# Kernel optimization log

Measured on AMD Instinct MI355X. Metric: run time of the kernel, lower is better.

Reference implementation:

```python
import jax, jax.numpy as jnp
import numpy as np

WIN = 7       # window_size (square)
SHIFT = 3     # shift_size
HEADS = 4
WS = WIN * WIN  # 49 tokens per window


def _rel_index():
    # Swin relative position index, shape (WS*WS,), static ints
    coords = np.stack(np.meshgrid(np.arange(WIN), np.arange(WIN), indexing='ij'))
    cf = coords.reshape(2, -1)
    rel = (cf[:, :, None] - cf[:, None, :]).transpose(1, 2, 0)  # (WS, WS, 2)
    rel[:, :, 0] += WIN - 1
    rel[:, :, 1] += WIN - 1
    rel[:, :, 0] *= 2 * WIN - 1
    return rel.sum(-1).reshape(-1)

_REL_IDX = jnp.asarray(_rel_index())


def _attn_mask(H, W):
    # shift mask per window, shape (num_windows, WS, WS), static
    m = np.zeros((H, W), np.float32)
    cnt = 0
    for h in ((0, -WIN), (-WIN, -SHIFT), (-SHIFT, None)):
        for w in ((0, -WIN), (-WIN, -SHIFT), (-SHIFT, None)):
            m[h[0]:h[1], w[0]:w[1]] = cnt
            cnt += 1
    m = m.reshape(H // WIN, WIN, W // WIN, WIN).transpose(0, 2, 1, 3).reshape(-1, WS)
    diff = m[:, None, :] - m[:, :, None]
    return np.where(diff == 0, 0.0, -100.0).astype(np.float32)


def setup_inputs() -> dict:
    key = jax.random.key(0)
    ks = jax.random.split(key, 6)
    C = 128
    return {
        'x': jax.random.normal(ks[0], (64, 56, 56, C), jnp.float32),
        'qkv_kernel': jax.random.normal(ks[1], (C, 3 * C), jnp.float32) * (C ** -0.5),
        'qkv_bias': jax.random.normal(ks[2], (3 * C,), jnp.float32) * 0.02,
        'proj_kernel': jax.random.normal(ks[3], (C, C), jnp.float32) * (C ** -0.5),
        'proj_bias': jax.random.normal(ks[4], (C,), jnp.float32) * 0.02,
        'rel_pos_table': jax.random.normal(ks[5], ((2 * WIN - 1) ** 2, HEADS), jnp.float32) * 0.02,
    }


def reference(x, qkv_kernel, qkv_bias, proj_kernel, proj_bias, rel_pos_table):
    B, H, W, C = x.shape
    nH, nW = H // WIN, W // WIN
    head_dim = C // HEADS

    # cyclic shift + window partition -> (B*nH*nW, WS, C)
    xs = jnp.roll(x, (-SHIFT, -SHIFT), axis=(1, 2))
    xw = xs.reshape(B, nH, WIN, nW, WIN, C).transpose(0, 1, 3, 2, 4, 5).reshape(B * nH * nW, WS, C)

    qkv = xw @ qkv_kernel + qkv_bias
    qkv = qkv.reshape(-1, WS, 3, HEADS, head_dim).transpose(2, 0, 3, 1, 4)  # (3, n, h, WS, d)
    q, k, v = qkv[0], qkv[1], qkv[2]

    attn = jnp.einsum('nhsd,nhtd->nhst', q * head_dim ** -0.5, k)

    # relative position bias: (1, heads, WS, WS)
    bias = rel_pos_table[_REL_IDX].reshape(WS, WS, HEADS).transpose(2, 0, 1)[None]
    attn = attn + bias

    # shift mask (static)
    mask = jnp.asarray(_attn_mask(H, W))  # (nH*nW, WS, WS)
    attn = attn.reshape(B, nH * nW, HEADS, WS, WS) + mask[None, :, None]
    attn = jax.nn.softmax(attn.reshape(-1, HEADS, WS, WS), axis=-1)

    out = jnp.einsum('nhst,nhtd->nhsd', attn, v).transpose(0, 2, 1, 3).reshape(-1, WS, C)
    out = out @ proj_kernel + proj_bias

    # window merge + reverse shift
    out = out.reshape(B, nH, nW, WIN, WIN, C).transpose(0, 1, 3, 2, 4, 5).reshape(B, H, W, C)
    return jnp.roll(out, (SHIFT, SHIFT), axis=(1, 2))
```

## Files before the change

kernel.cpp:

```cpp
#include <hip/hip_runtime.h>
#include <hip/hip_bf16.h>

#define WIN 7
#define SHIFT_SZ 3
#define WSQ 49
#define CH 128
#define HW 56
#define LOG2E 1.4426950408889634f
#define QSCALE (0.17677669529663687f * LOG2E)

typedef short s16x8 __attribute__((ext_vector_type(8)));
typedef short s16x4 __attribute__((ext_vector_type(4)));
typedef float f32x4 __attribute__((ext_vector_type(4)));

static __device__ __forceinline__ f32x4 mfma16(s16x4 a, s16x4 b, f32x4 c) {
#if __has_builtin(__builtin_amdgcn_mfma_f32_16x16x16bf16_1k)
  return __builtin_amdgcn_mfma_f32_16x16x16bf16_1k(a, b, c, 0, 0, 0);
#else
  f32x4 d;
  asm("v_mfma_f32_16x16x16_bf16 %0, %1, %2, %3" : "=v"(d) : "v"(a), "v"(b), "v"(c));
  return d;
#endif
}


__global__ void prep_weights(const float* __restrict__ qkv_kernel,
                             const float* __restrict__ proj_kernel,
                             __hip_bfloat16* __restrict__ ws) {
  int idx = blockIdx.x * 256 + threadIdx.x;
  if (idx < 49152) {
    int n = idx >> 7, c = idx & 127;
    ws[idx] = __float2bfloat16(qkv_kernel[c * 384 + n]);
  }
  if (idx < 16384) {
    int n = idx >> 7, c = idx & 127;
    ws[49152 + idx] = __float2bfloat16(proj_kernel[c * 128 + n]);
  }
}

__global__ void prep_tbl(const float* __restrict__ rel_pos_table,
                         __hip_bfloat16* __restrict__ tbl) {
  int idx = blockIdx.x * 256 + threadIdx.x;
  int t = idx & 63;
  int s = (idx >> 6) & 63;
  int h = (idx >> 12) & 3;
  int win = idx >> 14;
  float v;
  if (t >= WSQ) v = -43280.f;
  else if (s >= WSQ) v = 0.f;
  else {
    int i1 = s / 7, j1 = s % 7, i2 = t / 7, j2 = t % 7;
    int ridx = (i1 - i2 + 6) * 13 + (j1 - j2 + 6);
    float bias = rel_pos_table[ridx * 4 + h];
    int wy = win >> 3, wx = win & 7;
    int rh1 = (wy < 7) ? 0 : (i1 < 4 ? 1 : 2);
    int rh2 = (wy < 7) ? 0 : (i2 < 4 ? 1 : 2);
    int rw1 = (wx < 7) ? 0 : (j1 < 4 ? 1 : 2);
    int rw2 = (wx < 7) ? 0 : (j2 < 4 ? 1 : 2);
    float mask = (rh1 == rh2 && rw1 == rw2) ? 0.f : -100.f;
    v = (bias + mask) * LOG2E;
  }
  tbl[idx] = __float2bfloat16(v);
}


__launch_bounds__(512, 6)
__global__ void swin_attn(const float* __restrict__ x,
                          const float* __restrict__ qkv_bias,
                          const float* __restrict__ proj_bias,
                          const __hip_bfloat16* __restrict__ wqkvT,
                          const __hip_bfloat16* __restrict__ wprojT,
                          const __hip_bfloat16* __restrict__ tbl,
                          float* __restrict__ out) {
  __shared__ __align__(16) char smem[35840];
  __hip_bfloat16* a_lds  = (__hip_bfloat16*)smem;
  __hip_bfloat16* vt_lds = (__hip_bfloat16*)smem;
  __hip_bfloat16* k_lds  = (__hip_bfloat16*)(smem + 17408);
  __hip_bfloat16* o_lds  = (__hip_bfloat16*)(smem + 17408);

  const int tid = threadIdx.x;
  const int lane = tid & 63;
  const int wv = tid >> 6;
  const int g = lane >> 4;
  const int c = lane & 15;

  const int widx = blockIdx.x;
  const int b  = widx >> 6;
  const int wy = (widx >> 3) & 7;
  const int wx = widx & 7;
  const int win64 = widx & 63;

  const int h3 = wv >> 1;
  const int mh = wv & 1;

  for (int it = tid; it < 1024; it += 512) {
    int s = it >> 4;
    int l16 = it & 15;
    union { s16x8 v; __hip_bfloat16 h[8]; } u;
    if (s < WSQ) {
      int i = s / 7, j = s - i * 7;
      int hh = wy * 7 + i + SHIFT_SZ; if (hh >= HW) hh -= HW;
      int ww = wx * 7 + j + SHIFT_SZ; if (ww >= HW) ww -= HW;
      const float4* src = (const float4*)(x + (((b * HW + hh) * HW + ww) * CH + l16 * 8));
      float4 f0 = src[0], f1 = src[1];
      u.h[0] = __float2bfloat16(f0.x); u.h[1] = __float2bfloat16(f0.y);
      u.h[2] = __float2bfloat16(f0.z); u.h[3] = __float2bfloat16(f0.w);
      u.h[4] = __float2bfloat16(f1.x); u.h[5] = __float2bfloat16(f1.y);
      u.h[6] = __float2bfloat16(f1.z); u.h[7] = __float2bfloat16(f1.w);
    } else {
      #pragma unroll
      for (int q = 0; q < 8; ++q) u.h[q] = __float2bfloat16(0.f);
    }
    *(s16x8*)(a_lds + s * 136 + l16 * 8) = u.v;
  }
  __syncthreads();

  {
    f32x4 acc[4];
    #pragma unroll
    for (int mt = 0; mt < 4; ++mt) acc[mt] = (f32x4){0.f, 0.f, 0.f, 0.f};
    #pragma unroll
    for (int kt = 0; kt < 4; ++kt) {
      s16x8 bf = *(const s16x8*)(wqkvT + (16 * (8 + wv) + c) * 128 + kt * 32 + g * 8);
      #pragma unroll
      for (int mt = 0; mt < 4; ++mt) {
        s16x8 af = *(const s16x8*)(a_lds + (16 * mt + c) * 136 + kt * 32 + g * 8);
        acc[mt] = __builtin_amdgcn_mfma_f32_16x16x32_bf16(bf, af, acc[mt], 0, 0, 0);
      }
    }
    float4 kb4 = *(const float4*)(qkv_bias + 128 + 16 * wv + 4 * g);
    __hip_bfloat16* dst = k_lds + (wv >> 1) * 2304 + (wv & 1) * 16 + 4 * g;
    #pragma unroll
    for (int mt = 0; mt < 4; ++mt) {
      union { s16x4 v; __hip_bfloat16 h[4]; } u;
      u.h[0] = __float2bfloat16(acc[mt][0] + kb4.x);
      u.h[1] = __float2bfloat16(acc[mt][1] + kb4.y);
      u.h[2] = __float2bfloat16(acc[mt][2] + kb4.z);
      u.h[3] = __float2bfloat16(acc[mt][3] + kb4.w);
      *(s16x4*)(dst + (16 * mt + c) * 36) = u.v;
    }
  }

  s16x4 vheld[4];
  {
    f32x4 acc[4];
    #pragma unroll
    for (int mt = 0; mt < 4; ++mt) acc[mt] = (f32x4){0.f, 0.f, 0.f, 0.f};
    #pragma unroll
    for (int kt = 0; kt < 4; ++kt) {
      s16x8 bv = *(const s16x8*)(wqkvT + (16 * (16 + wv) + c) * 128 + kt * 32 + g * 8);
      #pragma unroll
      for (int mt = 0; mt < 4; ++mt) {
        s16x8 af = *(const s16x8*)(a_lds + (16 * mt + c) * 136 + kt * 32 + g * 8);
        acc[mt] = __builtin_amdgcn_mfma_f32_16x16x32_bf16(af, bv, acc[mt], 0, 0, 0);
      }
    }
    float vb = qkv_bias[256 + 16 * wv + c];
    #pragma unroll
    for (int mt = 0; mt < 4; ++mt) {
      union { s16x4 v; __hip_bfloat16 h[4]; } u;
      #pragma unroll
      for (int r = 0; r < 4; ++r) u.h[r] = __float2bfloat16(acc[mt][r] + vb);
      vheld[mt] = u.v;
    }
  }

  s16x4 qf16[2][2];
  {
    f32x4 acc[2][2];
    #pragma unroll
    for (int ntl = 0; ntl < 2; ++ntl)
      #pragma unroll
      for (int m = 0; m < 2; ++m) acc[ntl][m] = (f32x4){0.f, 0.f, 0.f, 0.f};
    #pragma unroll
    for (int kt = 0; kt < 4; ++kt) {
      s16x8 afq[2];
      #pragma unroll
      for (int m = 0; m < 2; ++m)
        afq[m] = *(const s16x8*)(a_lds + (16 * (2 * mh + m) + c) * 136 + kt * 32 + g * 8);
      #pragma unroll
      for (int ntl = 0; ntl < 2; ++ntl) {
        s16x8 bf = *(const s16x8*)(wqkvT + (16 * (2 * h3 + ntl) + c) * 128 + kt * 32 + g * 8);
        #pragma unroll
        for (int m = 0; m < 2; ++m)
          acc[ntl][m] = __builtin_amdgcn_mfma_f32_16x16x32_bf16(bf, afq[m], acc[ntl][m], 0, 0, 0);
      }
    }
    #pragma unroll
    for (int ntl = 0; ntl < 2; ++ntl) {
      float4 qb4 = *(const float4*)(qkv_bias + 32 * h3 + 16 * ntl + 4 * g);
      #pragma unroll
      for (int m = 0; m < 2; ++m) {
        union { s16x4 v; __hip_bfloat16 h[4]; } u;
        u.h[0] = __float2bfloat16((acc[ntl][m][0] + qb4.x) * QSCALE);
        u.h[1] = __float2bfloat16((acc[ntl][m][1] + qb4.y) * QSCALE);
        u.h[2] = __float2bfloat16((acc[ntl][m][2] + qb4.z) * QSCALE);
        u.h[3] = __float2bfloat16((acc[ntl][m][3] + qb4.w) * QSCALE);
        qf16[ntl][m] = u.v;
      }
    }
  }
  __syncthreads();

  {
    int row = (wv >> 1) * 32 + (wv & 1) * 16 + c;
    #pragma unroll
    for (int mt = 0; mt < 4; ++mt) {
      int tb = (4 * mt + g) ^ c;
      *(s16x4*)(vt_lds + row * 64 + tb * 4) = vheld[mt];
    }
  }

  s16x4 pf16[2][4];
  #pragma unroll
  for (int m = 0; m < 2; ++m) {
    f32x4 sc[4];
    #pragma unroll
    for (int nt = 0; nt < 4; ++nt) {
      sc[nt] = (f32x4){0.f, 0.f, 0.f, 0.f};
      #pragma unroll
      for (int kb = 0; kb < 2; ++kb) {
        s16x4 kf = *(const s16x4*)(k_lds + h3 * 2304 + (16 * nt + c) * 36 + 16 * kb + 4 * g);
        sc[nt] = mfma16(kf, qf16[kb][m], sc[nt]);
      }
    }
    const __hip_bfloat16* tb_ =
        tbl + (((win64 << 2) + h3) << 12) + (32 * mh + 16 * m + c) * 64;
    #pragma unroll
    for (int nt = 0; nt < 4; ++nt) {
      union { s16x4 v; __hip_bfloat16 h[4]; } tv;
      tv.v = *(const s16x4*)(tb_ + 16 * nt + 4 * g);
      #pragma unroll
      for (int r = 0; r < 4; ++r) sc[nt][r] += __bfloat162float(tv.h[r]);
    }
    float mx = -1e30f;
    #pragma unroll
    for (int nt = 0; nt < 4; ++nt)
      #pragma unroll
      for (int r = 0; r < 4; ++r) mx = fmaxf(mx, sc[nt][r]);
    mx = fmaxf(mx, __shfl_xor(mx, 16));
    mx = fmaxf(mx, __shfl_xor(mx, 32));
    float sum = 0.f;
    #pragma unroll
    for (int nt = 0; nt < 4; ++nt)
      #pragma unroll
      for (int r = 0; r < 4; ++r) {
        float e = __builtin_amdgcn_exp2f(sc[nt][r] - mx);
        sc[nt][r] = e;
        sum += e;
      }
    sum += __shfl_xor(sum, 16);
    sum += __shfl_xor(sum, 32);
    float inv = __builtin_amdgcn_rcpf(sum);
    #pragma unroll
    for (int nt = 0; nt < 4; ++nt) {
      union { s16x4 v; __hip_bfloat16 h[4]; } u;
      #pragma unroll
      for (int r = 0; r < 4; ++r) u.h[r] = __float2bfloat16(sc[nt][r] * inv);
      pf16[m][nt] = u.v;
    }
  }
  __syncthreads();

  f32x4 oacc[2][2];
  #pragma unroll
  for (int ntd = 0; ntd < 2; ++ntd) {
    s16x4 vf16[4];
    #pragma unroll
    for (int nt = 0; nt < 4; ++nt) {
      int row = h3 * 32 + 16 * ntd + c;
      int tb = (4 * nt + g) ^ c;
      vf16[nt] = *(const s16x4*)(vt_lds + row * 64 + tb * 4);
    }
    #pragma unroll
    for (int m = 0; m < 2; ++m) {
      oacc[m][ntd] = (f32x4){0.f, 0.f, 0.f, 0.f};
      #pragma unroll
      for (int nt = 0; nt < 4; ++nt)
        oacc[m][ntd] = mfma16(vf16[nt], pf16[m][nt], oacc[m][ntd]);
    }
  }
  #pragma unroll
  for (int m = 0; m < 2; ++m)
    #pragma unroll
    for (int ntd = 0; ntd < 2; ++ntd) {
      union { s16x4 v; __hip_bfloat16 h[4]; } u;
      #pragma unroll
      for (int r = 0; r < 4; ++r) u.h[r] = __float2bfloat16(oacc[m][ntd][r]);
      *(s16x4*)(o_lds + (32 * mh + 16 * m + c) * 136 + 32 * h3 + 16 * ntd + 4 * g) = u.v;
    }
  __syncthreads();

  {
    f32x4 pacc[4];
    #pragma unroll
    for (int mt = 0; mt < 4; ++mt) pacc[mt] = (f32x4){0.f, 0.f, 0.f, 0.f};
    #pragma unroll
    for (int kt = 0; kt < 4; ++kt) {
      s16x8 bfp = *(const s16x8*)(wprojT + (16 * wv + c) * 128 + kt * 32 + g * 8);
      #pragma unroll
      for (int mt = 0; mt < 4; ++mt) {
        s16x8 afo = *(const s16x8*)(o_lds + (16 * mt + c) * 136 + kt * 32 + g * 8);
        pacc[mt] = __builtin_amdgcn_mfma_f32_16x16x32_bf16(bfp, afo, pacc[mt], 0, 0, 0);
      }
    }
    float4 pb4 = *(const float4*)(proj_bias + 16 * wv + 4 * g);
    #pragma unroll
    for (int mt = 0; mt < 4; ++mt) {
      int s = 16 * mt + c;
      if (s < WSQ) {
        int i = s / 7, j = s - i * 7;
        int hh = wy * 7 + i + SHIFT_SZ; if (hh >= HW) hh -= HW;
        int ww = wx * 7 + j + SHIFT_SZ; if (ww >= HW) ww -= HW;
        float4 v;
        v.x = pacc[mt][0] + pb4.x;
        v.y = pacc[mt][1] + pb4.y;
        v.z = pacc[mt][2] + pb4.z;
        v.w = pacc[mt][3] + pb4.w;
        *(float4*)(out + ((b * HW + hh) * HW + ww) * CH + 16 * wv + 4 * g) = v;
      }
    }
  }
}

extern "C" void kernel_launch(void* const* d_in, const int* in_sizes, int n_in,
                              void* d_out, int out_size, void* d_ws, size_t ws_size,
                              hipStream_t stream) {
  const float* x            = (const float*)d_in[0];
  const float* qkv_kernel   = (const float*)d_in[1];
  const float* qkv_bias     = (const float*)d_in[2];
  const float* proj_kernel  = (const float*)d_in[3];
  const float* proj_bias    = (const float*)d_in[4];
  const float* rel_pos_tbl  = (const float*)d_in[5];
  float* out = (float*)d_out;

  __hip_bfloat16* wsb    = (__hip_bfloat16*)d_ws;
  __hip_bfloat16* wqkvT  = wsb;
  __hip_bfloat16* wprojT = wsb + 49152;
  __hip_bfloat16* tbl    = wsb + 65536;

  prep_weights<<<dim3(192), dim3(256), 0, stream>>>(qkv_kernel, proj_kernel, wsb);
  prep_tbl<<<dim3(4096), dim3(256), 0, stream>>>(rel_pos_tbl, tbl);
  swin_attn<<<dim3(4096), dim3(512), 0, stream>>>(x, qkv_bias, proj_bias,
                                                  wqkvT, wprojT, tbl, out);
}
```

Baseline: 140.9 us.

## Compute K and V redundantly per wave in registers, drop LDS staging and syncs

Each wave now computes the full K and V projections for its own head directly into registers, instead of splitting K/V across waves and exchanging them through LDS. This removes the K and V^T LDS buffers, two barriers and the LDS reads in the score and PV loops. In exchange, K and V projection MFMA work is done twice (by both waves of a head pair) and register pressure rises, which could hurt occupancy under the 512x6 launch bounds.

```diff
diff --git a/kernel.cpp b/kernel.cpp
--- a/kernel.cpp
+++ b/kernel.cpp
@@ -72,11 +72,9 @@
                           const __hip_bfloat16* __restrict__ wprojT,
                           const __hip_bfloat16* __restrict__ tbl,
                           float* __restrict__ out) {
-  __shared__ __align__(16) char smem[35840];
-  __hip_bfloat16* a_lds  = (__hip_bfloat16*)smem;
-  __hip_bfloat16* vt_lds = (__hip_bfloat16*)smem;
-  __hip_bfloat16* k_lds  = (__hip_bfloat16*)(smem + 17408);
-  __hip_bfloat16* o_lds  = (__hip_bfloat16*)(smem + 17408);
+  __shared__ __align__(16) char smem[34816];
+  __hip_bfloat16* a_lds = (__hip_bfloat16*)smem;
+  __hip_bfloat16* o_lds = (__hip_bfloat16*)(smem + 17408);
 
   const int tid = threadIdx.x;
   const int lane = tid & 63;
@@ -115,53 +113,39 @@
   }
   __syncthreads();
 
+  s16x4 kf16[2][4];
   {
-    f32x4 acc[4];
-    #pragma unroll
-    for (int mt = 0; mt < 4; ++mt) acc[mt] = (f32x4){0.f, 0.f, 0.f, 0.f};
+    f32x4 acc[2][4];
+    #pragma unroll
+    for (int kb = 0; kb < 2; ++kb)
+      #pragma unroll
+      for (int mt = 0; mt < 4; ++mt) acc[kb][mt] = (f32x4){0.f, 0.f, 0.f, 0.f};
     #pragma unroll
     for (int kt = 0; kt < 4; ++kt) {
-      s16x8 bf = *(const s16x8*)(wqkvT + (16 * (8 + wv) + c) * 128 + kt * 32 + g * 8);
+      s16x8 af[4];
+      #pragma unroll
+      for (int mt = 0; mt < 4; ++mt)
+        af[mt] = *(const s16x8*)(a_lds + (16 * mt + c) * 136 + kt * 32 + g * 8);
+      #pragma unroll
+      for (int kb = 0; kb < 2; ++kb) {
+        s16x8 bf = *(const s16x8*)(wqkvT + (128 + 32 * h3 + 16 * kb + c) * 128 + kt * 32 + g * 8);
+        #pragma unroll
+        for (int mt = 0; mt < 4; ++mt)
+          acc[kb][mt] = __builtin_amdgcn_mfma_f32_16x16x32_bf16(bf, af[mt], acc[kb][mt], 0, 0, 0);
+      }
+    }
+    #pragma unroll
+    for (int kb = 0; kb < 2; ++kb) {
+      float4 kb4 = *(const float4*)(qkv_bias + 128 + 32 * h3 + 16 * kb + 4 * g);
       #pragma unroll
       for (int mt = 0; mt < 4; ++mt) {
-        s16x8 af = *(const s16x8*)(a_lds + (16 * mt + c) * 136 + kt * 32 + g * 8);
-        acc[mt] = __builtin_amdgcn_mfma_f32_16x16x32_bf16(bf, af, acc[mt], 0, 0, 0);
-      }
-    }
-    float4 kb4 = *(const float4*)(qkv_bias + 128 + 16 * wv + 4 * g);
-    __hip_bfloat16* dst = k_lds + (wv >> 1) * 2304 + (wv & 1) * 16 + 4 * g;
-    #pragma unroll
-    for (int mt = 0; mt < 4; ++mt) {
-      union { s16x4 v; __hip_bfloat16 h[4]; } u;
-      u.h[0] = __float2bfloat16(acc[mt][0] + kb4.x);
-      u.h[1] = __float2bfloat16(acc[mt][1] + kb4.y);
-      u.h[2] = __float2bfloat16(acc[mt][2] + kb4.z);
-      u.h[3] = __float2bfloat16(acc[mt][3] + kb4.w);
-      *(s16x4*)(dst + (16 * mt + c) * 36) = u.v;
-    }
-  }
-
-  s16x4 vheld[4];
-  {
-    f32x4 acc[4];
-    #pragma unroll
-    for (int mt = 0; mt < 4; ++mt) acc[mt] = (f32x4){0.f, 0.f, 0.f, 0.f};
-    #pragma unroll
-    for (int kt = 0; kt < 4; ++kt) {
-      s16x8 bv = *(const s16x8*)(wqkvT + (16 * (16 + wv) + c) * 128 + kt * 32 + g * 8);
-      #pragma unroll
-      for (int mt = 0; mt < 4; ++mt) {
-        s16x8 af = *(const s16x8*)(a_lds + (16 * mt + c) * 136 + kt * 32 + g * 8);
-        acc[mt] = __builtin_amdgcn_mfma_f32_16x16x32_bf16(af, bv, acc[mt], 0, 0, 0);
-      }
-    }
-    float vb = qkv_bias[256 + 16 * wv + c];
-    #pragma unroll
-    for (int mt = 0; mt < 4; ++mt) {
-      union { s16x4 v; __hip_bfloat16 h[4]; } u;
-      #pragma unroll
-      for (int r = 0; r < 4; ++r) u.h[r] = __float2bfloat16(acc[mt][r] + vb);
-      vheld[mt] = u.v;
+        union { s16x4 v; __hip_bfloat16 h[4]; } u;
+        u.h[0] = __float2bfloat16(acc[kb][mt][0] + kb4.x);
+        u.h[1] = __float2bfloat16(acc[kb][mt][1] + kb4.y);
+        u.h[2] = __float2bfloat16(acc[kb][mt][2] + kb4.z);
+        u.h[3] = __float2bfloat16(acc[kb][mt][3] + kb4.w);
+        kf16[kb][mt] = u.v;
+      }
     }
   }
 
@@ -169,9 +153,9 @@
   {
     f32x4 acc[2][2];
     #pragma unroll
-    for (int ntl = 0; ntl < 2; ++ntl)
-      #pragma unroll
-      for (int m = 0; m < 2; ++m) acc[ntl][m] = (f32x4){0.f, 0.f, 0.f, 0.f};
+    for (int kb = 0; kb < 2; ++kb)
+      #pragma unroll
+      for (int m = 0; m < 2; ++m) acc[kb][m] = (f32x4){0.f, 0.f, 0.f, 0.f};
     #pragma unroll
     for (int kt = 0; kt < 4; ++kt) {
       s16x8 afq[2];
@@ -179,35 +163,25 @@
       for (int m = 0; m < 2; ++m)
         afq[m] = *(const s16x8*)(a_lds + (16 * (2 * mh + m) + c) * 136 + kt * 32 + g * 8);
       #pragma unroll
-      for (int ntl = 0; ntl < 2; ++ntl) {
-        s16x8 bf = *(const s16x8*)(wqkvT + (16 * (2 * h3 + ntl) + c) * 128 + kt * 32 + g * 8);
+      for (int kb = 0; kb < 2; ++kb) {
+        s16x8 bf = *(const s16x8*)(wqkvT + (32 * h3 + 16 * kb + c) * 128 + kt * 32 + g * 8);
         #pragma unroll
         for (int m = 0; m < 2; ++m)
-          acc[ntl][m] = __builtin_amdgcn_mfma_f32_16x16x32_bf16(bf, afq[m], acc[ntl][m], 0, 0, 0);
-      }
-    }
-    #pragma unroll
-    for (int ntl = 0; ntl < 2; ++ntl) {
-      float4 qb4 = *(const float4*)(qkv_bias + 32 * h3 + 16 * ntl + 4 * g);
+          acc[kb][m] = __builtin_amdgcn_mfma_f32_16x16x32_bf16(bf, afq[m], acc[kb][m], 0, 0, 0);
+      }
+    }
+    #pragma unroll
+    for (int kb = 0; kb < 2; ++kb) {
+      float4 qb4 = *(const float4*)(qkv_bias + 32 * h3 + 16 * kb + 4 * g);
       #pragma unroll
       for (int m = 0; m < 2; ++m) {
         union { s16x4 v; __hip_bfloat16 h[4]; } u;
-        u.h[0] = __float2bfloat16((acc[ntl][m][0] + qb4.x) * QSCALE);
-        u.h[1] = __float2bfloat16((acc[ntl][m][1] + qb4.y) * QSCALE);
-        u.h[2] = __float2bfloat16((acc[ntl][m][2] + qb4.z) * QSCALE);
-        u.h[3] = __float2bfloat16((acc[ntl][m][3] + qb4.w) * QSCALE);
-        qf16[ntl][m] = u.v;
-      }
-    }
-  }
-  __syncthreads();
-
-  {
-    int row = (wv >> 1) * 32 + (wv & 1) * 16 + c;
-    #pragma unroll
-    for (int mt = 0; mt < 4; ++mt) {
-      int tb = (4 * mt + g) ^ c;
-      *(s16x4*)(vt_lds + row * 64 + tb * 4) = vheld[mt];
+        u.h[0] = __float2bfloat16((acc[kb][m][0] + qb4.x) * QSCALE);
+        u.h[1] = __float2bfloat16((acc[kb][m][1] + qb4.y) * QSCALE);
+        u.h[2] = __float2bfloat16((acc[kb][m][2] + qb4.z) * QSCALE);
+        u.h[3] = __float2bfloat16((acc[kb][m][3] + qb4.w) * QSCALE);
+        qf16[kb][m] = u.v;
+      }
     }
   }
 
@@ -219,10 +193,8 @@
     for (int nt = 0; nt < 4; ++nt) {
       sc[nt] = (f32x4){0.f, 0.f, 0.f, 0.f};
       #pragma unroll
-      for (int kb = 0; kb < 2; ++kb) {
-        s16x4 kf = *(const s16x4*)(k_lds + h3 * 2304 + (16 * nt + c) * 36 + 16 * kb + 4 * g);
-        sc[nt] = mfma16(kf, qf16[kb][m], sc[nt]);
-      }
+      for (int kb = 0; kb < 2; ++kb)
+        sc[nt] = mfma16(kf16[kb][nt], qf16[kb][m], sc[nt]);
     }
     const __hip_bfloat16* tb_ =
         tbl + (((win64 << 2) + h3) << 12) + (32 * mh + 16 * m + c) * 64;
@@ -260,34 +232,53 @@
       pf16[m][nt] = u.v;
     }
   }
-  __syncthreads();
-
-  f32x4 oacc[2][2];
-  #pragma unroll
-  for (int ntd = 0; ntd < 2; ++ntd) {
-    s16x4 vf16[4];
-    #pragma unroll
-    for (int nt = 0; nt < 4; ++nt) {
-      int row = h3 * 32 + 16 * ntd + c;
-      int tb = (4 * nt + g) ^ c;
-      vf16[nt] = *(const s16x4*)(vt_lds + row * 64 + tb * 4);
-    }
-    #pragma unroll
-    for (int m = 0; m < 2; ++m) {
-      oacc[m][ntd] = (f32x4){0.f, 0.f, 0.f, 0.f};
-      #pragma unroll
-      for (int nt = 0; nt < 4; ++nt)
-        oacc[m][ntd] = mfma16(vf16[nt], pf16[m][nt], oacc[m][ntd]);
-    }
-  }
+
+  s16x4 vf16[2][4];
+  {
+    f32x4 acc[2][4];
+    #pragma unroll
+    for (int vt = 0; vt < 2; ++vt)
+      #pragma unroll
+      for (int mt = 0; mt < 4; ++mt) acc[vt][mt] = (f32x4){0.f, 0.f, 0.f, 0.f};
+    #pragma unroll
+    for (int kt = 0; kt < 4; ++kt) {
+      s16x8 af[4];
+      #pragma unroll
+      for (int mt = 0; mt < 4; ++mt)
+        af[mt] = *(const s16x8*)(a_lds + (16 * mt + c) * 136 + kt * 32 + g * 8);
+      #pragma unroll
+      for (int vt = 0; vt < 2; ++vt) {
+        s16x8 bv = *(const s16x8*)(wqkvT + (256 + 32 * h3 + 16 * vt + c) * 128 + kt * 32 + g * 8);
+        #pragma unroll
+        for (int mt = 0; mt < 4; ++mt)
+          acc[vt][mt] = __builtin_amdgcn_mfma_f32_16x16x32_bf16(af[mt], bv, acc[vt][mt], 0, 0, 0);
+      }
+    }
+    #pragma unroll
+    for (int vt = 0; vt < 2; ++vt) {
+      float vb = qkv_bias[256 + 32 * h3 + 16 * vt + c];
+      #pragma unroll
+      for (int mt = 0; mt < 4; ++mt) {
+        union { s16x4 v; __hip_bfloat16 h[4]; } u;
+        #pragma unroll
+        for (int r = 0; r < 4; ++r) u.h[r] = __float2bfloat16(acc[vt][mt][r] + vb);
+        vf16[vt][mt] = u.v;
+      }
+    }
+  }
+
   #pragma unroll
   for (int m = 0; m < 2; ++m)
     #pragma unroll
-    for (int ntd = 0; ntd < 2; ++ntd) {
+    for (int vt = 0; vt < 2; ++vt) {
+      f32x4 oacc = (f32x4){0.f, 0.f, 0.f, 0.f};
+      #pragma unroll
+      for (int nt = 0; nt < 4; ++nt)
+        oacc = mfma16(vf16[vt][nt], pf16[m][nt], oacc);
       union { s16x4 v; __hip_bfloat16 h[4]; } u;
       #pragma unroll
-      for (int r = 0; r < 4; ++r) u.h[r] = __float2bfloat16(oacc[m][ntd][r]);
-      *(s16x4*)(o_lds + (32 * mh + 16 * m + c) * 136 + 32 * h3 + 16 * ntd + 4 * g) = u.v;
+      for (int r = 0; r < 4; ++r) u.h[r] = __float2bfloat16(oacc[r]);
+      *(s16x4*)(o_lds + (32 * mh + 16 * m + c) * 136 + 32 * h3 + 16 * vt + 4 * g) = u.v;
     }
   __syncthreads();
 
```

After: 440.7 us. 3.13x slower.
